# Kernel optimization log

Measured on AMD Instinct MI355X. Metric: run time of the kernel, lower is better.

The kernel has to match this reference:

```python
import jax, jax.numpy as jnp
import numpy as np

H = 1024
V = 2048
B = 256
S = 512
SOS = 129
NSTEPS = 6


def setup_inputs() -> dict:
    key = jax.random.key(0)
    ks = jax.random.split(key, 16)
    sc = 0.05
    return {
        "encoder_outputs": jax.random.normal(ks[0], (B, S, H), jnp.float32),
        "h0": jax.random.normal(ks[1], (1, B, H), jnp.float32),
        "c0": jax.random.normal(ks[2], (1, B, H), jnp.float32),
        "embedding": jax.random.normal(ks[3], (V, H), jnp.float32) * sc,
        "W_ih": jax.random.normal(ks[4], (4 * H, H), jnp.float32) * sc,
        "W_hh": jax.random.normal(ks[5], (4 * H, H), jnp.float32) * sc,
        "b_ih": jax.random.normal(ks[6], (4 * H,), jnp.float32) * sc,
        "b_hh": jax.random.normal(ks[7], (4 * H,), jnp.float32) * sc,
        "attn_W": jax.random.normal(ks[8], (H, H), jnp.float32) * sc,
        "attn_b": jax.random.normal(ks[9], (H,), jnp.float32) * sc,
        "concat_W": jax.random.normal(ks[10], (H, 2 * H), jnp.float32) * sc,
        "concat_b": jax.random.normal(ks[11], (H,), jnp.float32) * sc,
        "lin_W": jax.random.normal(ks[12], (V, H), jnp.float32) * sc,
        "lin_b": jax.random.normal(ks[13], (V,), jnp.float32) * sc,
    }


def reference(encoder_outputs, h0, c0, embedding, W_ih, W_hh, b_ih, b_hh,
              attn_W, attn_b, concat_W, concat_b, lin_W, lin_b):
    enc = encoder_outputs  # [B, S, H]
    h = h0[0]  # [B, H] (n_layers = 1)
    c = c0[0]
    inp = jnp.full((B,), SOS, dtype=jnp.int32)  # decoder_input indices
    outs = []
    weights = None
    for _ in range(NSTEPS):
        # embedding lookup (dropout is identity in eval)
        x = embedding[inp]  # [B, H]
        # single LSTM step, PyTorch gate order i, f, g, o
        gates = x @ W_ih.T + b_ih + h @ W_hh.T + b_hh  # [B, 4H]
        i_g, f_g, g_g, o_g = jnp.split(gates, 4, axis=-1)
        c = jax.nn.sigmoid(f_g) * c + jax.nn.sigmoid(i_g) * jnp.tanh(g_g)
        h = jax.nn.sigmoid(o_g) * jnp.tanh(c)
        # Luong 'general' attention: softmax((W_a h) . enc)
        energy = h @ attn_W.T + attn_b  # [B, H]
        scores = jnp.einsum('bh,bsh->bs', energy, enc)  # [B, S]
        weights = jax.nn.softmax(scores, axis=-1)
        context = jnp.einsum('bs,bsh->bh', weights, enc)  # [B, H]
        cat = jnp.concatenate([h, context], axis=-1)  # [B, 2H]
        co = jnp.tanh(cat @ concat_W.T + concat_b)  # [B, H]
        logits = co @ lin_W.T + lin_b  # [B, V]
        outs.append(logits)
        # greedy next input (topk(1) ~ argmax), detached
        inp = jnp.argmax(logits, axis=-1).astype(jnp.int32)
    decoder_outputs = jnp.stack(outs, axis=1)  # [B, NSTEPS, V]
    return decoder_outputs, (h[None], c[None]), weights[:, None, :]
```

## Files before the change

### kernel.cpp

```cpp
#include <hip/hip_runtime.h>
#include <math.h>

#define HH 1024
#define VV 2048
#define BB 256
#define SS 512
#define NSTEPS 6
#define SOS 129

typedef __attribute__((ext_vector_type(8))) __bf16 bf16x8;
typedef __attribute__((ext_vector_type(4))) __bf16 bf16x4;
typedef __attribute__((ext_vector_type(2))) __bf16 bf16x2;
typedef __attribute__((ext_vector_type(4))) float f32x4;

__device__ __forceinline__ float sigmoidf_(float x) { return 1.0f / (1.0f + expf(-x)); }

__device__ __forceinline__ void split1(float x, __bf16& h, __bf16& l) {
  h = (__bf16)x;
  l = (__bf16)(x - (float)h);
}

__device__ __forceinline__ void gll16(const __bf16* src, __bf16* ldst) {
  __builtin_amdgcn_global_load_lds(
      (const __attribute__((address_space(1))) unsigned*)(const void*)src,
      (__attribute__((address_space(3))) unsigned*)(void*)ldst, 16, 0, 0);
}

template<int AMODE>
__global__ __launch_bounds__(256) void gemm3(
    const __bf16* __restrict__ Ah, const __bf16* __restrict__ Al, int lda,
    const __bf16* __restrict__ A1h, const __bf16* __restrict__ A1l,
    const int* __restrict__ aidx,
    const __bf16* __restrict__ Bh, const __bf16* __restrict__ Bl, int K,
    int kLen, float* __restrict__ P, int ldc,
    int ny, int nz)
{
  __shared__ __align__(16) __bf16 lds[2][4][64 * 64];
  const int t = threadIdx.x, lane = t & 63, wv = t >> 6;

  const int chunk = (int)(gridDim.x >> 3);
  const int w = (blockIdx.x & 7) * chunk + (blockIdx.x >> 3);
  const int bz = w % nz;
  const int by = (w / nz) % ny;
  const int bx = w / (nz * ny);

  const int row0 = by * 64, col0 = bx * 64;

  const int sslot = lane & 7;
  const int srw   = lane >> 3;
  int sw[2];
  const __bf16 *arh[2], *arl[2], *a1h[2], *a1l[2], *brh[2], *brl[2];
#pragma unroll
  for (int hf = 0; hf < 2; ++hf) {
    const int tr = wv * 16 + hf * 8 + srw;
    sw[hf] = (sslot ^ (tr & 7)) << 3;
    const int ar = row0 + tr;
    if (AMODE == 1) {
      const int r = aidx[ar];
      arh[hf] = Ah + (size_t)r * HH;
      arl[hf] = Al + (size_t)r * HH;
      a1h[hf] = A1h + (size_t)ar * 2048;
      a1l[hf] = A1l + (size_t)ar * 2048;
    } else {
      arh[hf] = Ah + (size_t)ar * lda;
      arl[hf] = Al + (size_t)ar * lda;
    }
    const int br = col0 + tr;
    brh[hf] = Bh + (size_t)br * K;
    brl[hf] = Bl + (size_t)br * K;
  }

  const int wr = (wv >> 1) * 32, wc = (wv & 1) * 32;
  const int fr = lane & 15, kb = (lane >> 4) * 8;

  const f32x4 fz = {0.f, 0.f, 0.f, 0.f};
  f32x4 acc[2][2] = {{fz, fz}, {fz, fz}};

  const int tBeg = (bz * kLen) >> 6;
  const int nt = kLen >> 6;

  auto stage = [&](int tIdx, int bi) {
    const int k0 = tIdx << 6;
#pragma unroll
    for (int hf = 0; hf < 2; ++hf) {
      const int rb = (wv * 16 + hf * 8) * 64;
      const __bf16 *sa_h, *sa_l;
      if (AMODE == 1 && k0 >= HH) {
        sa_h = a1h[hf] + (k0 - HH) + sw[hf];
        sa_l = a1l[hf] + (k0 - HH) + sw[hf];
      } else {
        sa_h = arh[hf] + k0 + sw[hf];
        sa_l = arl[hf] + k0 + sw[hf];
      }
      gll16(sa_h, &lds[bi][0][rb]);
      gll16(sa_l, &lds[bi][1][rb]);
      gll16(brh[hf] + k0 + sw[hf], &lds[bi][2][rb]);
      gll16(brl[hf] + k0 + sw[hf], &lds[bi][3][rb]);
    }
  };

  auto compute = [&](int bi) {
#pragma unroll
    for (int kc = 0; kc < 2; ++kc) {
      const int e = kc * 32 + kb;
      bf16x8 a_h[2], a_l[2], b_h[2], b_l[2];
#pragma unroll
      for (int i = 0; i < 2; ++i) {
        const int ra = wr + i * 16 + fr;
        const int ia = ra * 64 + (e ^ ((ra & 7) << 3));
        a_h[i] = *(const bf16x8*)&lds[bi][0][ia];
        a_l[i] = *(const bf16x8*)&lds[bi][1][ia];
        const int rb2 = wc + i * 16 + fr;
        const int ib = rb2 * 64 + (e ^ ((rb2 & 7) << 3));
        b_h[i] = *(const bf16x8*)&lds[bi][2][ib];
        b_l[i] = *(const bf16x8*)&lds[bi][3][ib];
      }
#pragma unroll
      for (int i = 0; i < 2; ++i)
#pragma unroll
        for (int j = 0; j < 2; ++j)
          acc[i][j] = __builtin_amdgcn_mfma_f32_16x16x32_bf16(a_h[i], b_h[j], acc[i][j], 0, 0, 0);
#pragma unroll
      for (int i = 0; i < 2; ++i)
#pragma unroll
        for (int j = 0; j < 2; ++j)
          acc[i][j] = __builtin_amdgcn_mfma_f32_16x16x32_bf16(a_h[i], b_l[j], acc[i][j], 0, 0, 0);
#pragma unroll
      for (int i = 0; i < 2; ++i)
#pragma unroll
        for (int j = 0; j < 2; ++j)
          acc[i][j] = __builtin_amdgcn_mfma_f32_16x16x32_bf16(a_l[i], b_h[j], acc[i][j], 0, 0, 0);
    }
  };

  stage(tBeg, 0);
  __syncthreads();
  int cur = 0;
  for (int tk = 0; tk < nt; ++tk) {
    if (tk + 1 < nt) stage(tBeg + tk + 1, cur ^ 1);
    compute(cur);
    __syncthreads();
    cur ^= 1;
  }

  float* Cp = P + (size_t)bz * 256 * ldc;
#pragma unroll
  for (int i = 0; i < 2; ++i)
#pragma unroll
    for (int j = 0; j < 2; ++j) {
      const int col = col0 + wc + j * 16 + fr;
#pragma unroll
      for (int r = 0; r < 4; ++r) {
        const int row = row0 + wr + i * 16 + (lane >> 4) * 4 + r;
        Cp[(size_t)row * ldc + col] = acc[i][j][r];
      }
    }
}

__global__ __launch_bounds__(256) void conv_all(
    const float* __restrict__ W_ih, const float* __restrict__ W_hh,
    const float* __restrict__ attn_W, const float* __restrict__ concat_W,
    const float* __restrict__ lin_W, const float* __restrict__ emb,
    __bf16* __restrict__ Wcat_h, __bf16* __restrict__ Wcat_l,
    __bf16* __restrict__ attnW_h, __bf16* __restrict__ attnW_l,
    __bf16* __restrict__ catW_h, __bf16* __restrict__ catW_l,
    __bf16* __restrict__ linW_h, __bf16* __restrict__ linW_l,
    __bf16* __restrict__ emb_h, __bf16* __restrict__ emb_l)
{
  const int i = blockIdx.x * 256 + threadIdx.x;
  const float* s;
  __bf16 *dh, *dl;
  size_t so, dofs;
  if (i < 2097152) {
    const int ii = i & 1048575;
    const int r = ii >> 8, cp = (ii & 255) << 2;
    s = (i < 1048576) ? W_ih : W_hh;
    so = (size_t)r * 1024 + cp;
    dh = Wcat_h; dl = Wcat_l;
    dofs = (size_t)r * 2048 + ((i < 1048576) ? 0 : 1024) + cp;
  } else if (i < 2359296) {
    const size_t ii = (size_t)(i - 2097152) << 2;
    s = attn_W; so = ii; dh = attnW_h; dl = attnW_l; dofs = ii;
  } else if (i < 2883584) {
    const size_t ii = (size_t)(i - 2359296) << 2;
    s = concat_W; so = ii; dh = catW_h; dl = catW_l; dofs = ii;
  } else if (i < 3407872) {
    const size_t ii = (size_t)(i - 2883584) << 2;
    s = lin_W; so = ii; dh = linW_h; dl = linW_l; dofs = ii;
  } else {
    const size_t ii = (size_t)(i - 3407872) << 2;
    s = emb; so = ii; dh = emb_h; dl = emb_l; dofs = ii;
  }
  const float4 v = *(const float4*)(s + so);
  __bf16 h0, l0, h1, l1, h2, l2, h3, l3;
  split1(v.x, h0, l0); split1(v.y, h1, l1); split1(v.z, h2, l2); split1(v.w, h3, l3);
  *(bf16x4*)&dh[dofs] = bf16x4{h0, h1, h2, h3};
  *(bf16x4*)&dl[dofs] = bf16x4{l0, l1, l2, l3};
}

__global__ __launch_bounds__(256) void lstm_reduce(
    const float* __restrict__ Pg, const float* __restrict__ bihh,
    float* c, float* h,
    __bf16* __restrict__ hcat_h, __bf16* __restrict__ hcat_l)
{
  const int id = blockIdx.x * 256 + threadIdx.x;
  const int b = id >> 10, j = id & 1023;
  const size_t base = (size_t)b * 4096 + j;
  const size_t cs = (size_t)256 * 4096;
  const float ig = Pg[base]        + Pg[base + cs]        + bihh[j];
  const float fg = Pg[base + 1024] + Pg[base + cs + 1024] + bihh[j + 1024];
  const float gg = Pg[base + 2048] + Pg[base + cs + 2048] + bihh[j + 2048];
  const float og = Pg[base + 3072] + Pg[base + cs + 3072] + bihh[j + 3072];
  const float cn = sigmoidf_(fg) * c[id] + sigmoidf_(ig) * tanhf(gg);
  const float hn = sigmoidf_(og) * tanhf(cn);
  c[id] = cn;
  h[id] = hn;
  __bf16 hh, hl;
  split1(hn, hh, hl);
  hcat_h[(size_t)b * 2048 + j] = hh;
  hcat_l[(size_t)b * 2048 + j] = hl;
}

__global__ __launch_bounds__(512) void attn_part(
    const float* __restrict__ Pe, const float* __restrict__ attn_b,
    const float* __restrict__ enc,
    float* __restrict__ pml, float* __restrict__ pcacc, float* __restrict__ scb)
{
  const int b = blockIdx.x >> 1, half = blockIdx.x & 1;
  const int base = half * 256;
  const int t = threadIdx.x, lane = t & 63, wv = t >> 6;
  __shared__ __align__(16) float ctxa[8][1024];
  __shared__ float wml[8][2];
  const float* encb = enc + (size_t)b * (SS * HH);

  f32x4 er[4];
  {
    const f32x4* P4 = (const f32x4*)Pe;
    const f32x4* B4 = (const f32x4*)attn_b;
#pragma unroll
    for (int i = 0; i < 4; ++i) {
      const size_t idx = (size_t)b * 256 + lane + 64 * i;
      f32x4 v = P4[idx];
      const f32x4 v1 = P4[idx + 65536], v2 = P4[idx + 131072], v3 = P4[idx + 196608];
      const f32x4 bb = B4[lane + 64 * i];
      v.x += v1.x + v2.x + v3.x + bb.x; v.y += v1.y + v2.y + v3.y + bb.y;
      v.z += v1.z + v2.z + v3.z + bb.z; v.w += v1.w + v2.w + v3.w + bb.w;
      er[i] = v;
    }
  }

  f32x4* cx = (f32x4*)ctxa[wv];
#pragma unroll
  for (int i = 0; i < 4; ++i) cx[lane + 64 * i] = f32x4{0.f, 0.f, 0.f, 0.f};

  float m = -INFINITY, lw = 0.0f;
  const int r0 = base + wv * 32;

  f32x4 r4[4];
  {
    const f32x4* row = (const f32x4*)(encb + (size_t)r0 * HH);
#pragma unroll
    for (int i = 0; i < 4; ++i) r4[i] = __builtin_nontemporal_load(&row[lane + 64 * i]);
  }

  for (int s = 0; s < 32; ++s) {
    f32x4 r4n[4];
    if (s + 1 < 32) {
      const f32x4* row = (const f32x4*)(encb + (size_t)(r0 + s + 1) * HH);
#pragma unroll
      for (int i = 0; i < 4; ++i) r4n[i] = __builtin_nontemporal_load(&row[lane + 64 * i]);
    }
    float p = 0.0f;
#pragma unroll
    for (int i = 0; i < 4; ++i)
      p += r4[i].x * er[i].x + r4[i].y * er[i].y + r4[i].z * er[i].z + r4[i].w * er[i].w;
#pragma unroll
    for (int off = 32; off; off >>= 1) p += __shfl_xor(p, off);
    if (lane == 0) scb[(size_t)b * SS + r0 + s] = p;

    if (p > m + 8.0f) {
      const float alpha = expf(m - p);
      lw *= alpha;
#pragma unroll
      for (int i = 0; i < 4; ++i) {
        f32x4 v = cx[lane + 64 * i];
        v.x *= alpha; v.y *= alpha; v.z *= alpha; v.w *= alpha;
        cx[lane + 64 * i] = v;
      }
      m = p;
    }
    const float e = expf(p - m);
    lw += e;
#pragma unroll
    for (int i = 0; i < 4; ++i) {
      f32x4 v = cx[lane + 64 * i];
      v.x += e * r4[i].x; v.y += e * r4[i].y; v.z += e * r4[i].z; v.w += e * r4[i].w;
      cx[lane + 64 * i] = v;
    }
#pragma unroll
    for (int i = 0; i < 4; ++i) r4[i] = r4n[i];
  }

  if (lane == 0) { wml[wv][0] = m; wml[wv][1] = lw; }
  __syncthreads();

  float M = -INFINITY;
#pragma unroll
  for (int w = 0; w < 8; ++w) M = fmaxf(M, wml[w][0]);
  float ew[8];
  float L = 0.0f;
#pragma unroll
  for (int w = 0; w < 8; ++w) { ew[w] = expf(wml[w][0] - M); L += wml[w][1] * ew[w]; }

  float2 acc = {0.0f, 0.0f};
#pragma unroll
  for (int w = 0; w < 8; ++w) {
    const float2 v = ((const float2*)ctxa[w])[t];
    acc.x += ew[w] * v.x; acc.y += ew[w] * v.y;
  }
  ((float2*)(pcacc + ((size_t)b * 2 + half) * HH))[t] = acc;
  if (t == 0) { pml[(b * 2 + half) * 2 + 0] = M; pml[(b * 2 + half) * 2 + 1] = L; }
}

__global__ __launch_bounds__(512) void attn_merge(
    const float* __restrict__ pml, const float* __restrict__ pcacc,
    const float* __restrict__ scb,
    __bf16* __restrict__ hcat_h, __bf16* __restrict__ hcat_l,
    float* __restrict__ wout)
{
  const int b = blockIdx.x, t = threadIdx.x;
  const float m0 = pml[b * 4 + 0], l0 = pml[b * 4 + 1];
  const float m1 = pml[b * 4 + 2], l1 = pml[b * 4 + 3];
  const float M = fmaxf(m0, m1);
  const float w0 = expf(m0 - M), w1 = expf(m1 - M);
  const float inv = 1.0f / (l0 * w0 + l1 * w1);
  const float2 c0 = ((const float2*)(pcacc + (size_t)b * 2048))[t];
  const float2 c1 = ((const float2*)(pcacc + (size_t)b * 2048 + 1024))[t];
  const float ox = (c0.x * w0 + c1.x * w1) * inv;
  const float oy = (c0.y * w0 + c1.y * w1) * inv;
  __bf16 h0, lo0, h1, lo1;
  split1(ox, h0, lo0); split1(oy, h1, lo1);
  const size_t ob = (size_t)b * 2048 + 1024 + 2 * t;
  *(bf16x2*)&hcat_h[ob] = bf16x2{h0, h1};
  *(bf16x2*)&hcat_l[ob] = bf16x2{lo0, lo1};
  wout[(size_t)b * SS + t] = expf(scb[(size_t)b * SS + t] - M) * inv;
}

__global__ __launch_bounds__(256) void co_reduce(
    const float* __restrict__ Pc, const float* __restrict__ concat_b,
    __bf16* __restrict__ co_h, __bf16* __restrict__ co_l)
{
  const int id = blockIdx.x * 256 + threadIdx.x;
  const size_t e4 = (size_t)id << 2;
  const int j = (int)(e4 & 1023);
  const size_t cs = (size_t)256 * 1024;
  float4 v = *(const float4*)(Pc + e4);
  const float4 v1 = *(const float4*)(Pc + e4 + cs);
  const float4 v2 = *(const float4*)(Pc + e4 + 2 * cs);
  const float4 v3 = *(const float4*)(Pc + e4 + 3 * cs);
  const float4 bb = *(const float4*)(concat_b + j);
  v.x = tanhf(v.x + v1.x + v2.x + v3.x + bb.x);
  v.y = tanhf(v.y + v1.y + v2.y + v3.y + bb.y);
  v.z = tanhf(v.z + v1.z + v2.z + v3.z + bb.z);
  v.w = tanhf(v.w + v1.w + v2.w + v3.w + bb.w);
  __bf16 h0, l0, h1, l1, h2, l2, h3, l3;
  split1(v.x, h0, l0); split1(v.y, h1, l1); split1(v.z, h2, l2); split1(v.w, h3, l3);
  *(bf16x4*)&co_h[e4] = bf16x4{h0, h1, h2, h3};
  *(bf16x4*)&co_l[e4] = bf16x4{l0, l1, l2, l3};
}

__global__ __launch_bounds__(256) void argmax_reduce(
    const float* __restrict__ Pl, const float* __restrict__ lin_b,
    float* __restrict__ dec, int coff, int* __restrict__ inp)
{
  const int b = blockIdx.x, t = threadIdx.x;
  const size_t rb = (size_t)b * 2048;
  const size_t cs = (size_t)256 * 2048;
  float* drow = dec + (size_t)b * (NSTEPS * VV) + coff;
  float best = -INFINITY; int bi = 0;
  for (int j = t; j < VV; j += 256) {
    const float v = Pl[rb + j] + Pl[rb + cs + j] + lin_b[j];
    drow[j] = v;
    if (v > best) { best = v; bi = j; }
  }
  __shared__ float vs[256];
  __shared__ int   is[256];
  vs[t] = best; is[t] = bi;
  __syncthreads();
  for (int stp = 128; stp; stp >>= 1) {
    if (t < stp) {
      const float v2 = vs[t + stp]; const int i2 = is[t + stp];
      if (v2 > vs[t] || (v2 == vs[t] && i2 < is[t])) { vs[t] = v2; is[t] = i2; }
    }
    __syncthreads();
  }
  if (t == 0) inp[b] = is[0];
}

__global__ __launch_bounds__(256) void init_kernel(
    const float* __restrict__ h0, const float* __restrict__ c0,
    float* h, float* c,
    const float* __restrict__ b_ih, const float* __restrict__ b_hh,
    float* bihh, int* inp,
    __bf16* __restrict__ hcat_h, __bf16* __restrict__ hcat_l)
{
  const int id = blockIdx.x * 256 + threadIdx.x;
  if (id < BB * HH) {
    const float hv = h0[id];
    h[id] = hv;
    c[id] = c0[id];
    __bf16 hh, hl;
    split1(hv, hh, hl);
    const int b = id >> 10, j = id & 1023;
    hcat_h[(size_t)b * 2048 + j] = hh;
    hcat_l[(size_t)b * 2048 + j] = hl;
  }
  if (id < 4096) bihh[id] = b_ih[id] + b_hh[id];
  if (id < BB) inp[id] = SOS;
}

extern "C" void kernel_launch(void* const* d_in, const int* in_sizes, int n_in,
                              void* d_out, int out_size, void* d_ws, size_t ws_size,
                              hipStream_t stream)
{
  (void)in_sizes; (void)n_in; (void)out_size; (void)ws_size;
  const float* enc      = (const float*)d_in[0];
  const float* h0       = (const float*)d_in[1];
  const float* c0       = (const float*)d_in[2];
  const float* emb      = (const float*)d_in[3];
  const float* W_ih     = (const float*)d_in[4];
  const float* W_hh     = (const float*)d_in[5];
  const float* b_ih     = (const float*)d_in[6];
  const float* b_hh     = (const float*)d_in[7];
  const float* attn_W   = (const float*)d_in[8];
  const float* attn_b   = (const float*)d_in[9];
  const float* concat_W = (const float*)d_in[10];
  const float* concat_b = (const float*)d_in[11];
  const float* lin_W    = (const float*)d_in[12];
  const float* lin_b    = (const float*)d_in[13];

  float* out = (float*)d_out;
  float* dec = out;
  float* h   = out + (size_t)BB * NSTEPS * VV;
  float* c   = h + (size_t)BB * HH;
  float* wts = c + (size_t)BB * HH;

  char* w = (char*)d_ws;
  auto alloc = [&](size_t bytes) { char* p = w; w += (bytes + 255) & ~255ull; return p; };
  float*  bihh    = (float*)alloc(4096 * 4);
  int*    inp     = (int*)alloc(BB * 4);
  __bf16* Wcat_h  = (__bf16*)alloc((size_t)4096 * 2048 * 2);
  __bf16* Wcat_l  = (__bf16*)alloc((size_t)4096 * 2048 * 2);
  __bf16* attnW_h = (__bf16*)alloc((size_t)1024 * 1024 * 2);
  __bf16* attnW_l = (__bf16*)alloc((size_t)1024 * 1024 * 2);
  __bf16* catW_h  = (__bf16*)alloc((size_t)1024 * 2048 * 2);
  __bf16* catW_l  = (__bf16*)alloc((size_t)1024 * 2048 * 2);
  __bf16* linW_h  = (__bf16*)alloc((size_t)2048 * 1024 * 2);
  __bf16* linW_l  = (__bf16*)alloc((size_t)2048 * 1024 * 2);
  __bf16* emb_h   = (__bf16*)alloc((size_t)VV * HH * 2);
  __bf16* emb_l   = (__bf16*)alloc((size_t)VV * HH * 2);
  __bf16* hcat_h  = (__bf16*)alloc((size_t)BB * 2048 * 2);
  __bf16* hcat_l  = (__bf16*)alloc((size_t)BB * 2048 * 2);
  __bf16* co_h    = (__bf16*)alloc((size_t)BB * 1024 * 2);
  __bf16* co_l    = (__bf16*)alloc((size_t)BB * 1024 * 2);
  float*  pml     = (float*)alloc(BB * 4 * 4);
  float*  pcacc   = (float*)alloc((size_t)BB * 2 * HH * 4);
  float*  scb     = (float*)alloc((size_t)BB * SS * 4);
  float*  Pg      = (float*)alloc((size_t)2 * BB * 4096 * 4);
  float*  Pe      = (float*)alloc((size_t)4 * BB * 1024 * 4);
  float*  Pc      = (float*)alloc((size_t)4 * BB * 1024 * 4);
  float*  Pl      = (float*)alloc((size_t)2 * BB * 2048 * 4);

  conv_all<<<15360, 256, 0, stream>>>(W_ih, W_hh, attn_W, concat_W, lin_W, emb,
                                      Wcat_h, Wcat_l, attnW_h, attnW_l,
                                      catW_h, catW_l, linW_h, linW_l, emb_h, emb_l);
  init_kernel<<<1024, 256, 0, stream>>>(h0, c0, h, c, b_ih, b_hh, bihh, inp,
                                        hcat_h, hcat_l);

  for (int step = 0; step < NSTEPS; ++step) {
    gemm3<1><<<512, 256, 0, stream>>>(
        emb_h, emb_l, HH, hcat_h, hcat_l, inp, Wcat_h, Wcat_l, 2048,
        1024, Pg, 4096, 4, 2);
    lstm_reduce<<<1024, 256, 0, stream>>>(Pg, bihh, c, h, hcat_h, hcat_l);
    gemm3<0><<<256, 256, 0, stream>>>(
        hcat_h, hcat_l, 2048, nullptr, nullptr, nullptr, attnW_h, attnW_l, 1024,
        256, Pe, 1024, 4, 4);
    attn_part<<<2 * BB, 512, 0, stream>>>(Pe, attn_b, enc, pml, pcacc, scb);
    attn_merge<<<BB, 512, 0, stream>>>(pml, pcacc, scb, hcat_h, hcat_l, wts);
    gemm3<0><<<256, 256, 0, stream>>>(
        hcat_h, hcat_l, 2048, nullptr, nullptr, nullptr, catW_h, catW_l, 2048,
        512, Pc, 1024, 4, 4);
    co_reduce<<<256, 256, 0, stream>>>(Pc, concat_b, co_h, co_l);
    gemm3<0><<<256, 256, 0, stream>>>(
        co_h, co_l, 1024, nullptr, nullptr, nullptr, linW_h, linW_l, 1024,
        512, Pl, 2048, 4, 2);
    argmax_reduce<<<BB, 256, 0, stream>>>(Pl, lin_b, dec, step * VV, inp);
  }
}
```

Baseline: 882.7 us.

## Fuse LSTM gates GEMM with cell update, merge attention halves, fuse concat epilogue

The gates GEMM now runs without split-K. Its weight rows are interleaved so each tile holds all four gates of the same hidden units, which lets the LSTM cell update run in the GEMM epilogue and removes the Pg round trip and the lstm_reduce kernel. Attention uses one block per batch row instead of two halves plus a merge kernel. The concat GEMM drops split-K and applies bias, tanh and the bf16 split in its epilogue, removing co_reduce. Double-buffered h buffers avoid read/write hazards. In exchange, the gates and concat GEMMs launch far fewer blocks (256 and 64) with longer K loops, and attention gets half the blocks, so GPU occupancy drops.

After: 956.0 us. 8.3% more time.

```diff
diff --git a/kernel.cpp b/kernel.cpp
--- a/kernel.cpp
+++ b/kernel.cpp
@@ -26,14 +26,14 @@
       (__attribute__((address_space(3))) unsigned*)(void*)ldst, 16, 0, 0);
 }
 
-template<int AMODE>
+template<int OMODE>
 __global__ __launch_bounds__(256) void gemm3(
     const __bf16* __restrict__ Ah, const __bf16* __restrict__ Al, int lda,
-    const __bf16* __restrict__ A1h, const __bf16* __restrict__ A1l,
-    const int* __restrict__ aidx,
     const __bf16* __restrict__ Bh, const __bf16* __restrict__ Bl, int K,
     int kLen, float* __restrict__ P, int ldc,
-    int ny, int nz)
+    int ny, int nz,
+    const float* __restrict__ bias,
+    __bf16* __restrict__ Ch, __bf16* __restrict__ Cl)
 {
   __shared__ __align__(16) __bf16 lds[2][4][64 * 64];
   const int t = threadIdx.x, lane = t & 63, wv = t >> 6;
@@ -43,28 +43,19 @@
   const int bz = w % nz;
   const int by = (w / nz) % ny;
   const int bx = w / (nz * ny);
-
   const int row0 = by * 64, col0 = bx * 64;
 
   const int sslot = lane & 7;
   const int srw   = lane >> 3;
   int sw[2];
-  const __bf16 *arh[2], *arl[2], *a1h[2], *a1l[2], *brh[2], *brl[2];
+  const __bf16 *arh[2], *arl[2], *brh[2], *brl[2];
 #pragma unroll
   for (int hf = 0; hf < 2; ++hf) {
     const int tr = wv * 16 + hf * 8 + srw;
     sw[hf] = (sslot ^ (tr & 7)) << 3;
     const int ar = row0 + tr;
-    if (AMODE == 1) {
-      const int r = aidx[ar];
-      arh[hf] = Ah + (size_t)r * HH;
-      arl[hf] = Al + (size_t)r * HH;
-      a1h[hf] = A1h + (size_t)ar * 2048;
-      a1l[hf] = A1l + (size_t)ar * 2048;
-    } else {
-      arh[hf] = Ah + (size_t)ar * lda;
-      arl[hf] = Al + (size_t)ar * lda;
-    }
+    arh[hf] = Ah + (size_t)ar * lda;
+    arl[hf] = Al + (size_t)ar * lda;
     const int br = col0 + tr;
     brh[hf] = Bh + (size_t)br * K;
     brl[hf] = Bl + (size_t)br * K;
@@ -84,16 +75,8 @@
 #pragma unroll
     for (int hf = 0; hf < 2; ++hf) {
       const int rb = (wv * 16 + hf * 8) * 64;
-      const __bf16 *sa_h, *sa_l;
-      if (AMODE == 1 && k0 >= HH) {
-        sa_h = a1h[hf] + (k0 - HH) + sw[hf];
-        sa_l = a1l[hf] + (k0 - HH) + sw[hf];
-      } else {
-        sa_h = arh[hf] + k0 + sw[hf];
-        sa_l = arl[hf] + k0 + sw[hf];
-      }
-      gll16(sa_h, &lds[bi][0][rb]);
-      gll16(sa_l, &lds[bi][1][rb]);
+      gll16(arh[hf] + k0 + sw[hf], &lds[bi][0][rb]);
+      gll16(arl[hf] + k0 + sw[hf], &lds[bi][1][rb]);
       gll16(brh[hf] + k0 + sw[hf], &lds[bi][2][rb]);
       gll16(brl[hf] + k0 + sw[hf], &lds[bi][3][rb]);
     }
@@ -143,18 +126,185 @@
     cur ^= 1;
   }
 
-  float* Cp = P + (size_t)bz * 256 * ldc;
+  if (OMODE == 0) {
+    float* Cp = P + (size_t)bz * 256 * ldc;
+#pragma unroll
+    for (int i = 0; i < 2; ++i)
+#pragma unroll
+      for (int j = 0; j < 2; ++j) {
+        const int col = col0 + wc + j * 16 + fr;
+#pragma unroll
+        for (int r = 0; r < 4; ++r) {
+          const int row = row0 + wr + i * 16 + (lane >> 4) * 4 + r;
+          Cp[(size_t)row * ldc + col] = acc[i][j][r];
+        }
+      }
+  } else {
+#pragma unroll
+    for (int i = 0; i < 2; ++i)
+#pragma unroll
+      for (int j = 0; j < 2; ++j) {
+        const int col = col0 + wc + j * 16 + fr;
+        const float bb = bias[col];
+#pragma unroll
+        for (int r = 0; r < 4; ++r) {
+          const int row = row0 + wr + i * 16 + (lane >> 4) * 4 + r;
+          const float v = tanhf(acc[i][j][r] + bb);
+          __bf16 vh, vl;
+          split1(v, vh, vl);
+          Ch[(size_t)row * ldc + col] = vh;
+          Cl[(size_t)row * ldc + col] = vl;
+        }
+      }
+  }
+}
+
+__global__ __launch_bounds__(256) void gates_lstm(
+    const __bf16* __restrict__ emb_h, const __bf16* __restrict__ emb_l,
+    const __bf16* __restrict__ hprev_h, const __bf16* __restrict__ hprev_l,
+    const int* __restrict__ aidx,
+    const __bf16* __restrict__ Bh, const __bf16* __restrict__ Bl,
+    const float* __restrict__ bihh,
+    float* __restrict__ c, float* __restrict__ h,
+    __bf16* __restrict__ hcur_h, __bf16* __restrict__ hcur_l)
+{
+  __shared__ __align__(16) __bf16 lds[2][4][64 * 64];
+  const int t = threadIdx.x, lane = t & 63, wv = t >> 6;
+
+  const int chunk = (int)(gridDim.x >> 3);
+  const int w = (blockIdx.x & 7) * chunk + (blockIdx.x >> 3);
+  const int by = w & 3;
+  const int bx = w >> 2;
+  const int row0 = by * 64, col0 = bx * 64;
+
+  const int sslot = lane & 7;
+  const int srw   = lane >> 3;
+  int sw[2];
+  const __bf16 *arh[2], *arl[2], *a1h[2], *a1l[2], *brh[2], *brl[2];
+#pragma unroll
+  for (int hf = 0; hf < 2; ++hf) {
+    const int tr = wv * 16 + hf * 8 + srw;
+    sw[hf] = (sslot ^ (tr & 7)) << 3;
+    const int ar = row0 + tr;
+    const int r = aidx[ar];
+    arh[hf] = emb_h + (size_t)r * HH;
+    arl[hf] = emb_l + (size_t)r * HH;
+    a1h[hf] = hprev_h + (size_t)ar * 2048;
+    a1l[hf] = hprev_l + (size_t)ar * 2048;
+    const int br = col0 + tr;
+    brh[hf] = Bh + (size_t)br * 2048;
+    brl[hf] = Bl + (size_t)br * 2048;
+  }
+
+  const int wr = (wv >> 1) * 32, wc = (wv & 1) * 32;
+  const int fr = lane & 15, kb = (lane >> 4) * 8;
+
+  const f32x4 fz = {0.f, 0.f, 0.f, 0.f};
+  f32x4 acc[2][2] = {{fz, fz}, {fz, fz}};
+
+  auto stage = [&](int tIdx, int bi) {
+    const int k0 = tIdx << 6;
+#pragma unroll
+    for (int hf = 0; hf < 2; ++hf) {
+      const int rb = (wv * 16 + hf * 8) * 64;
+      const __bf16 *sa_h, *sa_l;
+      if (k0 >= HH) {
+        sa_h = a1h[hf] + (k0 - HH) + sw[hf];
+        sa_l = a1l[hf] + (k0 - HH) + sw[hf];
+      } else {
+        sa_h = arh[hf] + k0 + sw[hf];
+        sa_l = arl[hf] + k0 + sw[hf];
+      }
+      gll16(sa_h, &lds[bi][0][rb]);
+      gll16(sa_l, &lds[bi][1][rb]);
+      gll16(brh[hf] + k0 + sw[hf], &lds[bi][2][rb]);
+      gll16(brl[hf] + k0 + sw[hf], &lds[bi][3][rb]);
+    }
+  };
+
+  auto compute = [&](int bi) {
+#pragma unroll
+    for (int kc = 0; kc < 2; ++kc) {
+      const int e = kc * 32 + kb;
+      bf16x8 a_h[2], a_l[2], b_h[2], b_l[2];
+#pragma unroll
+      for (int i = 0; i < 2; ++i) {
+        const int ra = wr + i * 16 + fr;
+        const int ia = ra * 64 + (e ^ ((ra & 7) << 3));
+        a_h[i] = *(const bf16x8*)&lds[bi][0][ia];
+        a_l[i] = *(const bf16x8*)&lds[bi][1][ia];
+        const int rb2 = wc + i * 16 + fr;
+        const int ib = rb2 * 64 + (e ^ ((rb2 & 7) << 3));
+        b_h[i] = *(const bf16x8*)&lds[bi][2][ib];
+        b_l[i] = *(const bf16x8*)&lds[bi][3][ib];
+      }
+#pragma unroll
+      for (int i = 0; i < 2; ++i)
+#pragma unroll
+        for (int j = 0; j < 2; ++j)
+          acc[i][j] = __builtin_amdgcn_mfma_f32_16x16x32_bf16(a_h[i], b_h[j], acc[i][j], 0, 0, 0);
+#pragma unroll
+      for (int i = 0; i < 2; ++i)
+#pragma unroll
+        for (int j = 0; j < 2; ++j)
+          acc[i][j] = __builtin_amdgcn_mfma_f32_16x16x32_bf16(a_h[i], b_l[j], acc[i][j], 0, 0, 0);
+#pragma unroll
+      for (int i = 0; i < 2; ++i)
+#pragma unroll
+        for (int j = 0; j < 2; ++j)
+          acc[i][j] = __builtin_amdgcn_mfma_f32_16x16x32_bf16(a_l[i], b_h[j], acc[i][j], 0, 0, 0);
+    }
+  };
+
+  stage(0, 0);
+  __syncthreads();
+  int cur = 0;
+  for (int tk = 0; tk < 32; ++tk) {
+    if (tk + 1 < 32) stage(tk + 1, cur ^ 1);
+    compute(cur);
+    __syncthreads();
+    cur ^= 1;
+  }
+
+  float (*sc)[68] = (float (*)[68])(&lds[0][0][0]);
 #pragma unroll
   for (int i = 0; i < 2; ++i)
 #pragma unroll
     for (int j = 0; j < 2; ++j) {
-      const int col = col0 + wc + j * 16 + fr;
+      const int cl = wc + j * 16 + fr;
+      const float bb = bihh[col0 + cl];
 #pragma unroll
       for (int r = 0; r < 4; ++r) {
-        const int row = row0 + wr + i * 16 + (lane >> 4) * 4 + r;
-        Cp[(size_t)row * ldc + col] = acc[i][j][r];
-      }
-    }
+        const int rl = wr + i * 16 + (lane >> 4) * 4 + r;
+        sc[rl][cl] = acc[i][j][r] + bb;
+      }
+    }
+  __syncthreads();
+
+  const int rl2 = t >> 2;
+  const int b2 = row0 + rl2;
+  const int u0 = (t & 3) << 2;
+  const int j0 = (col0 >> 2) + u0;
+  const float4 cv = *(const float4*)&c[b2 * 1024 + j0];
+  float cn[4], hn[4];
+#pragma unroll
+  for (int q = 0; q < 4; ++q) {
+    const int u = u0 + q;
+    const float ig = sc[rl2][u * 4 + 0];
+    const float fg = sc[rl2][u * 4 + 1];
+    const float gg = sc[rl2][u * 4 + 2];
+    const float og = sc[rl2][u * 4 + 3];
+    const float cold = (&cv.x)[q];
+    cn[q] = sigmoidf_(fg) * cold + sigmoidf_(ig) * tanhf(gg);
+    hn[q] = sigmoidf_(og) * tanhf(cn[q]);
+  }
+  *(float4*)&c[b2 * 1024 + j0] = float4{cn[0], cn[1], cn[2], cn[3]};
+  *(float4*)&h[b2 * 1024 + j0] = float4{hn[0], hn[1], hn[2], hn[3]};
+  __bf16 hh[4], hl[4];
+#pragma unroll
+  for (int q = 0; q < 4; ++q) split1(hn[q], hh[q], hl[q]);
+  *(bf16x4*)&hcur_h[(size_t)b2 * 2048 + j0] = bf16x4{hh[0], hh[1], hh[2], hh[3]};
+  *(bf16x4*)&hcur_l[(size_t)b2 * 2048 + j0] = bf16x4{hl[0], hl[1], hl[2], hl[3]};
 }
 
 __global__ __launch_bounds__(256) void conv_all(
@@ -177,7 +327,8 @@
     s = (i < 1048576) ? W_ih : W_hh;
     so = (size_t)r * 1024 + cp;
     dh = Wcat_h; dl = Wcat_l;
-    dofs = (size_t)r * 2048 + ((i < 1048576) ? 0 : 1024) + cp;
+    const int rr = ((r & 1023) << 2) | (r >> 10);
+    dofs = (size_t)rr * 2048 + ((i < 1048576) ? 0 : 1024) + cp;
   } else if (i < 2359296) {
     const size_t ii = (size_t)(i - 2097152) << 2;
     s = attn_W; so = ii; dh = attnW_h; dl = attnW_l; dofs = ii;
@@ -198,38 +349,16 @@
   *(bf16x4*)&dl[dofs] = bf16x4{l0, l1, l2, l3};
 }
 
-__global__ __launch_bounds__(256) void lstm_reduce(
-    const float* __restrict__ Pg, const float* __restrict__ bihh,
-    float* c, float* h,
-    __bf16* __restrict__ hcat_h, __bf16* __restrict__ hcat_l)
-{
-  const int id = blockIdx.x * 256 + threadIdx.x;
-  const int b = id >> 10, j = id & 1023;
-  const size_t base = (size_t)b * 4096 + j;
-  const size_t cs = (size_t)256 * 4096;
-  const float ig = Pg[base]        + Pg[base + cs]        + bihh[j];
-  const float fg = Pg[base + 1024] + Pg[base + cs + 1024] + bihh[j + 1024];
-  const float gg = Pg[base + 2048] + Pg[base + cs + 2048] + bihh[j + 2048];
-  const float og = Pg[base + 3072] + Pg[base + cs + 3072] + bihh[j + 3072];
-  const float cn = sigmoidf_(fg) * c[id] + sigmoidf_(ig) * tanhf(gg);
-  const float hn = sigmoidf_(og) * tanhf(cn);
-  c[id] = cn;
-  h[id] = hn;
-  __bf16 hh, hl;
-  split1(hn, hh, hl);
-  hcat_h[(size_t)b * 2048 + j] = hh;
-  hcat_l[(size_t)b * 2048 + j] = hl;
-}
-
-__global__ __launch_bounds__(512) void attn_part(
+__global__ __launch_bounds__(512) void attn_fused(
     const float* __restrict__ Pe, const float* __restrict__ attn_b,
     const float* __restrict__ enc,
-    float* __restrict__ pml, float* __restrict__ pcacc, float* __restrict__ scb)
-{
-  const int b = blockIdx.x >> 1, half = blockIdx.x & 1;
-  const int base = half * 256;
+    __bf16* __restrict__ hcur_h, __bf16* __restrict__ hcur_l,
+    float* __restrict__ wout)
+{
+  const int b = blockIdx.x;
   const int t = threadIdx.x, lane = t & 63, wv = t >> 6;
   __shared__ __align__(16) float ctxa[8][1024];
+  __shared__ float scl[SS];
   __shared__ float wml[8][2];
   const float* encb = enc + (size_t)b * (SS * HH);
 
@@ -254,7 +383,7 @@
   for (int i = 0; i < 4; ++i) cx[lane + 64 * i] = f32x4{0.f, 0.f, 0.f, 0.f};
 
   float m = -INFINITY, lw = 0.0f;
-  const int r0 = base + wv * 32;
+  const int r0 = wv * 64;
 
   f32x4 r4[4];
   {
@@ -263,9 +392,9 @@
     for (int i = 0; i < 4; ++i) r4[i] = __builtin_nontemporal_load(&row[lane + 64 * i]);
   }
 
-  for (int s = 0; s < 32; ++s) {
+  for (int s = 0; s < 64; ++s) {
     f32x4 r4n[4];
-    if (s + 1 < 32) {
+    if (s + 1 < 64) {
       const f32x4* row = (const f32x4*)(encb + (size_t)(r0 + s + 1) * HH);
 #pragma unroll
       for (int i = 0; i < 4; ++i) r4n[i] = __builtin_nontemporal_load(&row[lane + 64 * i]);
@@ -276,7 +405,7 @@
       p += r4[i].x * er[i].x + r4[i].y * er[i].y + r4[i].z * er[i].z + r4[i].w * er[i].w;
 #pragma unroll
     for (int off = 32; off; off >>= 1) p += __shfl_xor(p, off);
-    if (lane == 0) scb[(size_t)b * SS + r0 + s] = p;
+    if (lane == 0) scl[r0 + s] = p;
 
     if (p > m + 8.0f) {
       const float alpha = expf(m - p);
@@ -311,6 +440,7 @@
   float L = 0.0f;
 #pragma unroll
   for (int w = 0; w < 8; ++w) { ew[w] = expf(wml[w][0] - M); L += wml[w][1] * ew[w]; }
+  const float inv = 1.0f / L;
 
   float2 acc = {0.0f, 0.0f};
 #pragma unroll
@@ -318,55 +448,13 @@
     const float2 v = ((const float2*)ctxa[w])[t];
     acc.x += ew[w] * v.x; acc.y += ew[w] * v.y;
   }
-  ((float2*)(pcacc + ((size_t)b * 2 + half) * HH))[t] = acc;
-  if (t == 0) { pml[(b * 2 + half) * 2 + 0] = M; pml[(b * 2 + half) * 2 + 1] = L; }
-}
-
-__global__ __launch_bounds__(512) void attn_merge(
-    const float* __restrict__ pml, const float* __restrict__ pcacc,
-    const float* __restrict__ scb,
-    __bf16* __restrict__ hcat_h, __bf16* __restrict__ hcat_l,
-    float* __restrict__ wout)
-{
-  const int b = blockIdx.x, t = threadIdx.x;
-  const float m0 = pml[b * 4 + 0], l0 = pml[b * 4 + 1];
-  const float m1 = pml[b * 4 + 2], l1 = pml[b * 4 + 3];
-  const float M = fmaxf(m0, m1);
-  const float w0 = expf(m0 - M), w1 = expf(m1 - M);
-  const float inv = 1.0f / (l0 * w0 + l1 * w1);
-  const float2 c0 = ((const float2*)(pcacc + (size_t)b * 2048))[t];
-  const float2 c1 = ((const float2*)(pcacc + (size_t)b * 2048 + 1024))[t];
-  const float ox = (c0.x * w0 + c1.x * w1) * inv;
-  const float oy = (c0.y * w0 + c1.y * w1) * inv;
-  __bf16 h0, lo0, h1, lo1;
-  split1(ox, h0, lo0); split1(oy, h1, lo1);
+  const float ox = acc.x * inv, oy = acc.y * inv;
+  __bf16 h0b, lo0, h1b, lo1;
+  split1(ox, h0b, lo0); split1(oy, h1b, lo1);
   const size_t ob = (size_t)b * 2048 + 1024 + 2 * t;
-  *(bf16x2*)&hcat_h[ob] = bf16x2{h0, h1};
-  *(bf16x2*)&hcat_l[ob] = bf16x2{lo0, lo1};
-  wout[(size_t)b * SS + t] = expf(scb[(size_t)b * SS + t] - M) * inv;
-}
-
-__global__ __launch_bounds__(256) void co_reduce(
-    const float* __restrict__ Pc, const float* __restrict__ concat_b,
-    __bf16* __restrict__ co_h, __bf16* __restrict__ co_l)
-{
-  const int id = blockIdx.x * 256 + threadIdx.x;
-  const size_t e4 = (size_t)id << 2;
-  const int j = (int)(e4 & 1023);
-  const size_t cs = (size_t)256 * 1024;
-  float4 v = *(const float4*)(Pc + e4);
-  const float4 v1 = *(const float4*)(Pc + e4 + cs);
-  const float4 v2 = *(const float4*)(Pc + e4 + 2 * cs);
-  const float4 v3 = *(const float4*)(Pc + e4 + 3 * cs);
-  const float4 bb = *(const float4*)(concat_b + j);
-  v.x = tanhf(v.x + v1.x + v2.x + v3.x + bb.x);
-  v.y = tanhf(v.y + v1.y + v2.y + v3.y + bb.y);
-  v.z = tanhf(v.z + v1.z + v2.z + v3.z + bb.z);
-  v.w = tanhf(v.w + v1.w + v2.w + v3.w + bb.w);
-  __bf16 h0, l0, h1, l1, h2, l2, h3, l3;
-  split1(v.x, h0, l0); split1(v.y, h1, l1); split1(v.z, h2, l2); split1(v.w, h3, l3);
-  *(bf16x4*)&co_h[e4] = bf16x4{h0, h1, h2, h3};
-  *(bf16x4*)&co_l[e4] = bf16x4{l0, l1, l2, l3};
+  *(bf16x2*)&hcur_h[ob] = bf16x2{h0b, h1b};
+  *(bf16x2*)&hcur_l[ob] = bf16x2{lo0, lo1};
+  wout[(size_t)b * SS + t] = expf(scl[t] - M) * inv;
 }
 
 __global__ __launch_bounds__(256) void argmax_reduce(
@@ -402,7 +490,7 @@
     float* h, float* c,
     const float* __restrict__ b_ih, const float* __restrict__ b_hh,
     float* bihh, int* inp,
-    __bf16* __restrict__ hcat_h, __bf16* __restrict__ hcat_l)
+    __bf16* __restrict__ hprev_h, __bf16* __restrict__ hprev_l)
 {
   const int id = blockIdx.x * 256 + threadIdx.x;
   if (id < BB * HH) {
@@ -412,10 +500,10 @@
     __bf16 hh, hl;
     split1(hv, hh, hl);
     const int b = id >> 10, j = id & 1023;
-    hcat_h[(size_t)b * 2048 + j] = hh;
-    hcat_l[(size_t)b * 2048 + j] = hl;
-  }
-  if (id < 4096) bihh[id] = b_ih[id] + b_hh[id];
+    hprev_h[(size_t)b * 2048 + j] = hh;
+    hprev_l[(size_t)b * 2048 + j] = hl;
+  }
+  if (id < 4096) bihh[((id & 1023) << 2) | (id >> 10)] = b_ih[id] + b_hh[id];
   if (id < BB) inp[id] = SOS;
 }
 
@@ -459,41 +547,40 @@
   __bf16* linW_l  = (__bf16*)alloc((size_t)2048 * 1024 * 2);
   __bf16* emb_h   = (__bf16*)alloc((size_t)VV * HH * 2);
   __bf16* emb_l   = (__bf16*)alloc((size_t)VV * HH * 2);
-  __bf16* hcat_h  = (__bf16*)alloc((size_t)BB * 2048 * 2);
-  __bf16* hcat_l  = (__bf16*)alloc((size_t)BB * 2048 * 2);
+  __bf16* hcatA_h = (__bf16*)alloc((size_t)BB * 2048 * 2);
+  __bf16* hcatA_l = (__bf16*)alloc((size_t)BB * 2048 * 2);
+  __bf16* hcatB_h = (__bf16*)alloc((size_t)BB * 2048 * 2);
+  __bf16* hcatB_l = (__bf16*)alloc((size_t)BB * 2048 * 2);
   __bf16* co_h    = (__bf16*)alloc((size_t)BB * 1024 * 2);
   __bf16* co_l    = (__bf16*)alloc((size_t)BB * 1024 * 2);
-  float*  pml     = (float*)alloc(BB * 4 * 4);
-  float*  pcacc   = (float*)alloc((size_t)BB * 2 * HH * 4);
-  float*  scb     = (float*)alloc((size_t)BB * SS * 4);
-  float*  Pg      = (float*)alloc((size_t)2 * BB * 4096 * 4);
   float*  Pe      = (float*)alloc((size_t)4 * BB * 1024 * 4);
-  float*  Pc      = (float*)alloc((size_t)4 * BB * 1024 * 4);
   float*  Pl      = (float*)alloc((size_t)2 * BB * 2048 * 4);
 
   conv_all<<<15360, 256, 0, stream>>>(W_ih, W_hh, attn_W, concat_W, lin_W, emb,
                                       Wcat_h, Wcat_l, attnW_h, attnW_l,
                                       catW_h, catW_l, linW_h, linW_l, emb_h, emb_l);
   init_kernel<<<1024, 256, 0, stream>>>(h0, c0, h, c, b_ih, b_hh, bihh, inp,
-                                        hcat_h, hcat_l);
+                                        hcatA_h, hcatA_l);
 
   for (int step = 0; step < NSTEPS; ++step) {
-    gemm3<1><<<512, 256, 0, stream>>>(
-        emb_h, emb_l, HH, hcat_h, hcat_l, inp, Wcat_h, Wcat_l, 2048,
-        1024, Pg, 4096, 4, 2);
-    lstm_reduce<<<1024, 256, 0, stream>>>(Pg, bihh, c, h, hcat_h, hcat_l);
+    __bf16* hprev_h = (step & 1) ? hcatB_h : hcatA_h;
+    __bf16* hprev_l = (step & 1) ? hcatB_l : hcatA_l;
+    __bf16* hcur_h  = (step & 1) ? hcatA_h : hcatB_h;
+    __bf16* hcur_l  = (step & 1) ? hcatA_l : hcatB_l;
+
+    gates_lstm<<<256, 256, 0, stream>>>(
+        emb_h, emb_l, hprev_h, hprev_l, inp, Wcat_h, Wcat_l, bihh,
+        c, h, hcur_h, hcur_l);
     gemm3<0><<<256, 256, 0, stream>>>(
-        hcat_h, hcat_l, 2048, nullptr, nullptr, nullptr, attnW_h, attnW_l, 1024,
-        256, Pe, 1024, 4, 4);
-    attn_part<<<2 * BB, 512, 0, stream>>>(Pe, attn_b, enc, pml, pcacc, scb);
-    attn_merge<<<BB, 512, 0, stream>>>(pml, pcacc, scb, hcat_h, hcat_l, wts);
+        hcur_h, hcur_l, 2048, attnW_h, attnW_l, 1024,
+        256, Pe, 1024, 4, 4, nullptr, nullptr, nullptr);
+    attn_fused<<<BB, 512, 0, stream>>>(Pe, attn_b, enc, hcur_h, hcur_l, wts);
+    gemm3<1><<<64, 256, 0, stream>>>(
+        hcur_h, hcur_l, 2048, catW_h, catW_l, 2048,
+        2048, nullptr, 1024, 4, 1, concat_b, co_h, co_l);
     gemm3<0><<<256, 256, 0, stream>>>(
-        hcat_h, hcat_l, 2048, nullptr, nullptr, nullptr, catW_h, catW_l, 2048,
-        512, Pc, 1024, 4, 4);
-    co_reduce<<<256, 256, 0, stream>>>(Pc, concat_b, co_h, co_l);
-    gemm3<0><<<256, 256, 0, stream>>>(
-        co_h, co_l, 1024, nullptr, nullptr, nullptr, linW_h, linW_l, 1024,
-        512, Pl, 2048, 4, 2);
+        co_h, co_l, 1024, linW_h, linW_l, 1024,
+        512, Pl, 2048, 4, 2, nullptr, nullptr, nullptr);
     argmax_reduce<<<BB, 256, 0, stream>>>(Pl, lin_b, dec, step * VV, inp);
   }
 }
```
